# Performance work log

Measured on AMD Instinct MI355X. Metric: run time of the kernel, lower is better.

Reference implementation:

```python
import jax, jax.numpy as jnp
import numpy as np

B, A, M, N = 16, 98304, 32, 32  # batch, anchors, gt boxes per image, sample size
IMG = 512.0


def _make_boxes(key, prefix):
    """Valid [x1,y1,x2,y2] boxes inside a 512px image (x2>x1, y2>y1)."""
    k1, k2 = jax.random.split(key)
    xy = jax.random.uniform(k1, prefix + (2,), minval=0.0, maxval=IMG - 130.0)
    wh = jax.random.uniform(k2, prefix + (2,), minval=16.0, maxval=128.0)
    return jnp.concatenate([xy, xy + wh], axis=-1)


def setup_inputs() -> dict:
    key = jax.random.key(0)
    ks = jax.random.split(key, 4)
    classifications = jax.random.uniform(ks[0], (B, A, 2), minval=0.01, maxval=0.99)
    regressions = jax.random.normal(ks[1], (B, A, 4), dtype=jnp.float32)
    anchors = _make_boxes(ks[2], (1, A))
    ann_boxes = _make_boxes(ks[3], (B, M))
    annotations = jnp.concatenate([ann_boxes, jnp.zeros((B, M, 1))], axis=-1)
    w = jnp.ones((B, 4), dtype=jnp.float32)
    return {"classifications": classifications, "regressions": regressions,
            "anchors": anchors, "annotations": annotations, "w": w}


def _calc_iou(a, b):
    # a: [A,4] anchors, b: [M,4] gt boxes -> [A,M]
    area = (b[:, 2] - b[:, 0]) * (b[:, 3] - b[:, 1])  # [M]
    iw = jnp.minimum(a[:, 2:3], b[None, :, 2]) - jnp.maximum(a[:, 0:1], b[None, :, 0])
    ih = jnp.minimum(a[:, 3:4], b[None, :, 3]) - jnp.maximum(a[:, 1:2], b[None, :, 1])
    iw = jnp.clip(iw, 0.0)
    ih = jnp.clip(ih, 0.0)
    a_area = (a[:, 2] - a[:, 0]) * (a[:, 3] - a[:, 1])  # [A]
    ua = jnp.clip(a_area[:, None] + area[None, :] - iw * ih, 1e-8)
    return iw * ih / ua


def _per_image(cls_j, reg_j, anchor, ann_j, w_j, keys):
    nA = anchor.shape[0]
    cls_j = jnp.clip(cls_j, 1e-7, 1.0 - 1e-7)
    # class forced to 0, coords clamped to [0,512] (as in the torch module)
    bbox = jnp.clip(ann_j[:, :4], 0.0, IMG)
    iou = _calc_iou(anchor, bbox)                # [A, M]
    iou_max = iou.max(axis=1)
    iou_arg = iou.argmax(axis=1)

    # --- positive sampling: random subset of size min(N, count) via random top-k ---
    thresh = jnp.minimum(iou_max.max(), 0.7)
    pos_elig = iou_max >= thresh
    s_pos = jnp.where(pos_elig, jax.random.uniform(keys[0], (nA,), minval=0.1, maxval=1.0), -1.0)
    vpos, ipos = jax.lax.top_k(s_pos, N)
    keep_pos = vpos > 0.0                         # only eligible anchors
    pos_sel = jnp.zeros(nA, bool).at[ipos].set(keep_pos)
    K = keep_pos.sum()

    # --- negative sampling: random subset of size min(2N-K, count) ---
    neg_elig = (iou_max < 0.4) & (iou_max >= 0.1)
    s_neg = jnp.where(neg_elig, jax.random.uniform(keys[1], (nA,), minval=0.1, maxval=1.0), -1.0)
    vneg, ineg = jax.lax.top_k(s_neg, 2 * N)
    keep_neg = (vneg > 0.0) & (jnp.arange(2 * N) < (2 * N - K))
    neg_sel = jnp.zeros(nA, bool).at[ineg].set(keep_neg)

    # targets: positives -> [1,0] (class forced to 0), negatives -> [0,1], else -1 (ignore)
    t0 = jnp.where(pos_sel, 1.0, jnp.where(neg_sel, 0.0, -1.0))
    t1 = jnp.where(pos_sel, 0.0, jnp.where(neg_sel, 1.0, -1.0))
    targets = jnp.stack([t0, t1], axis=-1)       # [A,2]
    cls_loss = jnp.where(targets != -1.0, -(targets * jnp.log(cls_j)), 0.0).sum() / (2 * N)

    aw = anchor[:, 2] - anchor[:, 0]
    ah = anchor[:, 3] - anchor[:, 1]
    acx = anchor[:, 0] + 0.5 * aw
    acy = anchor[:, 1] + 0.5 * ah
    assigned = bbox[iou_arg]                     # [A,4]
    gw = assigned[:, 2] - assigned[:, 0]
    gh = assigned[:, 3] - assigned[:, 1]
    gcx = assigned[:, 0] + 0.5 * gw
    gcy = assigned[:, 1] + 0.5 * gh
    gw = jnp.maximum(gw, 1.0)
    gh = jnp.maximum(gh, 1.0)
    t = jnp.stack([(gcx - acx) / aw, (gcy - acy) / ah,
                   jnp.log(gw / aw), jnp.log(gh / ah)], axis=-1)
    t = t / jnp.array([0.1, 0.1, 0.2, 0.2], dtype=t.dtype)
    diff = jnp.abs(t - reg_j)
    sl1 = jnp.where(diff <= 1.0 / 9.0, 0.5 * 9.0 * diff * diff, diff - 0.5 / 9.0)
    reg_loss = (sl1 * pos_sel[:, None].astype(sl1.dtype)).sum() * w_j[0] / (2 * N)
    return cls_loss, reg_loss


def reference(classifications, regressions, anchors, annotations, w):
    anchor = anchors[0]
    bsz = classifications.shape[0]
    keys = jax.random.split(jax.random.key(42), bsz * 2).reshape(bsz, 2)
    cl, rl = jax.vmap(
        lambda c, r, a, wj, k: _per_image(c, r, anchor, a, wj, k)
    )(classifications, regressions, annotations, w, keys)
    return (jnp.mean(cl, keepdims=True), jnp.mean(rl, keepdims=True))
```

## Files before the change

kernel.cpp:

```cpp
#include <hip/hip_runtime.h>

#define NB 16
#define NA 98304
#define NM 32
#define NS 32
#define BLKI 48
#define BLKP 96
#define TARGET 256
#define GCAP 1024
#define BCAP 512

typedef unsigned int u32;
typedef unsigned long long u64;

static_assert(NA == BLKI * 256 * 8, "coverage iou");
static_assert(NA == BLKP * 256 * 4, "coverage push");

struct WS {
  u64   pos_key[NB * GCAP];
  u64   neg_key[NB * GCAP];
  float iou_max[NB * NA];
  float blk_max[NB * BLKI];
  int   blk_nneg[NB * BLKI];
  int   blk_npos[NB * BLKI];
  float thresh[NB], cut_pos[NB], cut_neg[NB];
  int   n_neg[NB], n_pos07[NB], ge07[NB];
  u32   keys[NB][4];
  int   pos_cnt[NB], neg_cnt[NB];
  u32   cls_bits[NB], reg_bits[NB];
  int   done;
};

__device__ __forceinline__ u32 rotl32(u32 v, int d) { return (v << d) | (v >> (32 - d)); }

__device__ __forceinline__ void threefry2x32(u32 k0, u32 k1, u32 x0, u32 x1, u32& o0, u32& o1) {
  u32 k2 = k0 ^ k1 ^ 0x1BD11BDAu;
  x0 += k0; x1 += k1;
  x0 += x1; x1 = rotl32(x1, 13); x1 ^= x0;
  x0 += x1; x1 = rotl32(x1, 15); x1 ^= x0;
  x0 += x1; x1 = rotl32(x1, 26); x1 ^= x0;
  x0 += x1; x1 = rotl32(x1, 6);  x1 ^= x0;
  x0 += k1; x1 += k2 + 1u;
  x0 += x1; x1 = rotl32(x1, 17); x1 ^= x0;
  x0 += x1; x1 = rotl32(x1, 29); x1 ^= x0;
  x0 += x1; x1 = rotl32(x1, 16); x1 ^= x0;
  x0 += x1; x1 = rotl32(x1, 24); x1 ^= x0;
  x0 += k2; x1 += k0 + 2u;
  x0 += x1; x1 = rotl32(x1, 13); x1 ^= x0;
  x0 += x1; x1 = rotl32(x1, 15); x1 ^= x0;
  x0 += x1; x1 = rotl32(x1, 26); x1 ^= x0;
  x0 += x1; x1 = rotl32(x1, 6);  x1 ^= x0;
  x0 += k0; x1 += k1 + 3u;
  x0 += x1; x1 = rotl32(x1, 17); x1 ^= x0;
  x0 += x1; x1 = rotl32(x1, 29); x1 ^= x0;
  x0 += x1; x1 = rotl32(x1, 16); x1 ^= x0;
  x0 += x1; x1 = rotl32(x1, 24); x1 ^= x0;
  x0 += k1; x1 += k2 + 4u;
  x0 += x1; x1 = rotl32(x1, 13); x1 ^= x0;
  x0 += x1; x1 = rotl32(x1, 15); x1 ^= x0;
  x0 += x1; x1 = rotl32(x1, 26); x1 ^= x0;
  x0 += x1; x1 = rotl32(x1, 6);  x1 ^= x0;
  x0 += k2; x1 += k0 + 5u;
  o0 = x0; o1 = x1;
}

__device__ __forceinline__ float tf_uniform(u32 k0, u32 k1, u32 idx) {
  u32 o0, o1;
  threefry2x32(k0, k1, 0u, idx, o0, o1);
  u32 bits = o0 ^ o1;
  float f = __uint_as_float((bits >> 9) | 0x3F800000u) - 1.0f;
  float u = __fadd_rn(__fmul_rn(f, (1.0f - 0.1f)), 0.1f);
  return fmaxf(0.1f, u);
}

__device__ __forceinline__ u64 pack_key(float u, u32 a) {
  return ((u64)__float_as_uint(u) << 32) | (u64)(u32)(~a);
}

__global__ __launch_bounds__(256) void k_iou(const float* __restrict__ anchors,
                                             const float* __restrict__ ann,
                                             WS* __restrict__ ws) {
  int b = blockIdx.y;
  int tid = threadIdx.x;
  int a0 = (blockIdx.x * 256 + tid) * 8;
  __shared__ float bx1[NM], by1[NM], bx2[NM], by2[NM], barea[NM];
  __shared__ float wmax[4];
  __shared__ int wneg[4], wpos[4];
  if (tid < NM) {
    int m = tid;
    const float* p = ann + ((size_t)b * NM + m) * 5;
    float x1 = fminf(fmaxf(p[0], 0.0f), 512.0f);
    float y1 = fminf(fmaxf(p[1], 0.0f), 512.0f);
    float x2 = fminf(fmaxf(p[2], 0.0f), 512.0f);
    float y2 = fminf(fmaxf(p[3], 0.0f), 512.0f);
    bx1[m] = x1; by1[m] = y1; bx2[m] = x2; by2[m] = y2;
    barea[m] = __fmul_rn(__fsub_rn(x2, x1), __fsub_rn(y2, y1));
  }
  __syncthreads();

  const float4* a4 = (const float4*)anchors;
  float4 ap[8];
  float aarea[8], bi[8], bu[8];
#pragma unroll
  for (int k = 0; k < 8; k++) {
    ap[k] = a4[a0 + k];
    aarea[k] = __fmul_rn(__fsub_rn(ap[k].z, ap[k].x), __fsub_rn(ap[k].w, ap[k].y));
    bi[k] = -1.0f;
    bu[k] = 1.0f;
  }
  for (int m = 0; m < NM; m++) {
    float x1 = bx1[m], y1 = by1[m], x2 = bx2[m], y2 = by2[m], ar = barea[m];
#pragma unroll
    for (int k = 0; k < 8; k++) {
      float iw = fmaxf(__fsub_rn(fminf(ap[k].z, x2), fmaxf(ap[k].x, x1)), 0.0f);
      float ih = fmaxf(__fsub_rn(fminf(ap[k].w, y2), fmaxf(ap[k].y, y1)), 0.0f);
      float inter = __fmul_rn(iw, ih);
      float ua = __fsub_rn(__fadd_rn(aarea[k], ar), inter);
      bool upd = __fmul_rn(inter, bu[k]) > __fmul_rn(bi[k], ua);
      bi[k] = upd ? inter : bi[k];
      bu[k] = upd ? ua : bu[k];
    }
  }
  float best[8];
#pragma unroll
  for (int k = 0; k < 8; k++) best[k] = __fdiv_rn(bi[k], bu[k]);

  size_t o = (size_t)b * NA + a0;
  *(float4*)&ws->iou_max[o]     = make_float4(best[0], best[1], best[2], best[3]);
  *(float4*)&ws->iou_max[o + 4] = make_float4(best[4], best[5], best[6], best[7]);

  float lmax = -1.0f;
  int cneg = 0, cpos = 0;
#pragma unroll
  for (int k = 0; k < 8; k++) {
    lmax = fmaxf(lmax, best[k]);
    cneg += (best[k] < 0.4f && best[k] >= 0.1f) ? 1 : 0;
    cpos += (best[k] >= 0.7f) ? 1 : 0;
  }
  for (int s = 32; s > 0; s >>= 1) {
    lmax = fmaxf(lmax, __shfl_xor(lmax, s));
    cneg += __shfl_xor(cneg, s);
    cpos += __shfl_xor(cpos, s);
  }
  int wid = tid >> 6;
  if ((tid & 63) == 0) { wmax[wid] = lmax; wneg[wid] = cneg; wpos[wid] = cpos; }
  __syncthreads();
  if (tid < 4) {
    lmax = wmax[tid]; cneg = wneg[tid]; cpos = wpos[tid];
    for (int s = 2; s > 0; s >>= 1) {
      lmax = fmaxf(lmax, __shfl_xor(lmax, s));
      cneg += __shfl_xor(cneg, s);
      cpos += __shfl_xor(cpos, s);
    }
    if (tid == 0) {
      int oo = b * BLKI + blockIdx.x;
      ws->blk_max[oo] = lmax;
      ws->blk_nneg[oo] = cneg;
      ws->blk_npos[oo] = cpos;
    }
  }
}

__global__ __launch_bounds__(256) void k_stats(WS* __restrict__ ws) {
  int tid = threadIdx.x;
  int b = tid >> 4, l = tid & 15;
  float m = -1.0f;
  int nn = 0, np = 0;
  for (int i = l; i < BLKI; i += 16) {
    m = fmaxf(m, ws->blk_max[b * BLKI + i]);
    nn += ws->blk_nneg[b * BLKI + i];
    np += ws->blk_npos[b * BLKI + i];
  }
  for (int s = 8; s > 0; s >>= 1) {
    m = fmaxf(m, __shfl_xor(m, s));
    nn += __shfl_xor(nn, s);
    np += __shfl_xor(np, s);
  }
  if (l == 0) {
    ws->thresh[b] = fminf(m, 0.7f);
    int ge = (m >= 0.7f) ? 1 : 0;
    ws->ge07[b] = ge;
    ws->n_neg[b] = nn;
    ws->n_pos07[b] = np;
    ws->cut_neg[b] = (nn <= TARGET) ? -1.0f : (1.0f - 0.9f * ((float)TARGET / (float)nn));
    ws->cut_pos[b] = (ge && np > TARGET) ? (1.0f - 0.9f * ((float)TARGET / (float)np)) : -1.0f;
    ws->pos_cnt[b] = 0;
    ws->neg_cnt[b] = 0;
    u32 o0, o1;
    threefry2x32(0u, 42u, 0u, (u32)(2 * b), o0, o1);
    ws->keys[b][0] = o0; ws->keys[b][1] = o1;
    threefry2x32(0u, 42u, 0u, (u32)(2 * b + 1), o0, o1);
    ws->keys[b][2] = o0; ws->keys[b][3] = o1;
  }
  if (tid == 0) ws->done = 0;
}

__global__ __launch_bounds__(256) void k_push(WS* __restrict__ ws) {
  int b = blockIdx.y, tid = threadIdx.x;
  int a0 = (blockIdx.x * 256 + tid) * 4;
  __shared__ u64 pbuf[BCAP], nbuf[BCAP];
  __shared__ int pcnt, ncnt, pbase, nbase;
  if (tid == 0) { pcnt = 0; ncnt = 0; }
  __syncthreads();
  float thresh = ws->thresh[b];
  float cp = ws->cut_pos[b], cn = ws->cut_neg[b];
  u32 k0 = ws->keys[b][0], k1 = ws->keys[b][1];
  u32 k2 = ws->keys[b][2], k3 = ws->keys[b][3];
  float4 im4 = *(const float4*)&ws->iou_max[(size_t)b * NA + a0];
  float imv[4] = {im4.x, im4.y, im4.z, im4.w};
#pragma unroll
  for (int k = 0; k < 4; k++) {
    float im = imv[k];
    u32 a = (u32)(a0 + k);
    if (im >= thresh) {
      float u = tf_uniform(k0, k1, a);
      if (u >= cp) {
        int p = atomicAdd(&pcnt, 1);
        if (p < BCAP) pbuf[p] = pack_key(u, a);
      }
    }
    if (im < 0.4f && im >= 0.1f) {
      float u = tf_uniform(k2, k3, a);
      if (u >= cn) {
        int p = atomicAdd(&ncnt, 1);
        if (p < BCAP) nbuf[p] = pack_key(u, a);
      }
    }
  }
  __syncthreads();
  if (tid == 0) {
    pbase = (pcnt > 0) ? atomicAdd(&ws->pos_cnt[b], pcnt) : 0;
    nbase = (ncnt > 0) ? atomicAdd(&ws->neg_cnt[b], ncnt) : 0;
  }
  __syncthreads();
  int pc = min(pcnt, BCAP), nc = min(ncnt, BCAP);
  for (int i = tid; i < pc; i += 256) { int g = pbase + i; if (g < GCAP) ws->pos_key[b * GCAP + g] = pbuf[i]; }
  for (int i = tid; i < nc; i += 256) { int g = nbase + i; if (g < GCAP) ws->neg_key[b * GCAP + g] = nbuf[i]; }
}

__global__ __launch_bounds__(256) void k_select(const float* __restrict__ cls,
                                                const float* __restrict__ reg,
                                                const float* __restrict__ anchors,
                                                const float* __restrict__ ann,
                                                const float* __restrict__ w,
                                                WS* __restrict__ ws,
                                                float* __restrict__ out) {
  int b = blockIdx.x, tid = threadIdx.x;
  __shared__ u64 pk[GCAP], nk[GCAP];
  __shared__ float bx1[NM], by1[NM], bx2[NM], by2[NM], barea[NM];
  __shared__ int selp[NS], seln[2 * NS];
  __shared__ float tpos[NS], treg[NS], tneg[2 * NS];

  if (tid < NM) {
    int m = tid;
    const float* p = ann + ((size_t)b * NM + m) * 5;
    float x1 = fminf(fmaxf(p[0], 0.0f), 512.0f);
    float y1 = fminf(fmaxf(p[1], 0.0f), 512.0f);
    float x2 = fminf(fmaxf(p[2], 0.0f), 512.0f);
    float y2 = fminf(fmaxf(p[3], 0.0f), 512.0f);
    bx1[m] = x1; by1[m] = y1; bx2[m] = x2; by2[m] = y2;
    barea[m] = __fmul_rn(__fsub_rn(x2, x1), __fsub_rn(y2, y1));
  }

  int mp = min(ws->pos_cnt[b], GCAP);
  int mn = min(ws->neg_cnt[b], GCAP);
  int n_pos = ws->ge07[b] ? ws->n_pos07[b] : ws->pos_cnt[b];
  int n_neg = ws->n_neg[b];
  int K = min(NS, n_pos);
  int rp = min(K, mp);
  int rn = min(min(2 * NS - K, n_neg), mn);

  int mpad = (mp + 255) & ~255;
  int npad = (mn + 255) & ~255;
  for (int i = tid; i < mpad; i += 256) pk[i] = (i < mp) ? ws->pos_key[b * GCAP + i] : 0ull;
  for (int i = tid; i < npad; i += 256) nk[i] = (i < mn) ? ws->neg_key[b * GCAP + i] : 0ull;
  if (tid < NS) { tpos[tid] = 0.0f; treg[tid] = 0.0f; }
  if (tid < 2 * NS) tneg[tid] = 0.0f;
  __syncthreads();

  {
    u64 ck[GCAP / 256]; int cr[GCAP / 256];
    int nc = mpad >> 8;
#pragma unroll
    for (int c = 0; c < GCAP / 256; c++) { ck[c] = 0; cr[c] = 0; }
    for (int c = 0; c < nc; c++) ck[c] = pk[tid + (c << 8)];
    for (int j = 0; j < mp; j++) {
      u64 v = pk[j];
#pragma unroll
      for (int c = 0; c < GCAP / 256; c++) cr[c] += (v > ck[c]) ? 1 : 0;
    }
    for (int c = 0; c < nc; c++)
      if (ck[c] != 0 && cr[c] < rp) selp[cr[c]] = (int)(~(u32)ck[c]);
  }
  {
    u64 ck[GCAP / 256]; int cr[GCAP / 256];
    int nc = npad >> 8;
#pragma unroll
    for (int c = 0; c < GCAP / 256; c++) { ck[c] = 0; cr[c] = 0; }
    for (int c = 0; c < nc; c++) ck[c] = nk[tid + (c << 8)];
    for (int j = 0; j < mn; j++) {
      u64 v = nk[j];
#pragma unroll
      for (int c = 0; c < GCAP / 256; c++) cr[c] += (v > ck[c]) ? 1 : 0;
    }
    for (int c = 0; c < nc; c++)
      if (ck[c] != 0 && cr[c] < rn) seln[cr[c]] = (int)(~(u32)ck[c]);
  }
  __syncthreads();

  const float PLO = 1e-7f;
  const float PHI = (float)(1.0 - 1e-7);
  if (tid < rp) {
    int a = selp[tid];
    float p = cls[((size_t)b * NA + a) * 2 + 0];
    p = fminf(fmaxf(p, PLO), PHI);
    tpos[tid] = -logf(p);
    float4 apf = ((const float4*)anchors)[a];
    float ax1 = apf.x, ay1 = apf.y, ax2 = apf.z, ay2 = apf.w;
    float aarea = __fmul_rn(__fsub_rn(ax2, ax1), __fsub_rn(ay2, ay1));
    float bestv = -1.0f; int bestm = 0;
    for (int m = 0; m < NM; m++) {
      float iw = fmaxf(__fsub_rn(fminf(ax2, bx2[m]), fmaxf(ax1, bx1[m])), 0.0f);
      float ih = fmaxf(__fsub_rn(fminf(ay2, by2[m]), fmaxf(ay1, by1[m])), 0.0f);
      float inter = __fmul_rn(iw, ih);
      float ua = fmaxf(__fsub_rn(__fadd_rn(aarea, barea[m]), inter), 1e-8f);
      float v = __fdiv_rn(inter, ua);
      if (v > bestv) { bestv = v; bestm = m; }
    }
    float aw_ = __fsub_rn(ax2, ax1), ah_ = __fsub_rn(ay2, ay1);
    float acx = __fadd_rn(ax1, __fmul_rn(0.5f, aw_));
    float acy = __fadd_rn(ay1, __fmul_rn(0.5f, ah_));
    float gx1 = bx1[bestm], gy1 = by1[bestm], gx2 = bx2[bestm], gy2 = by2[bestm];
    float gw = __fsub_rn(gx2, gx1), gh = __fsub_rn(gy2, gy1);
    float gcx = __fadd_rn(gx1, __fmul_rn(0.5f, gw));
    float gcy = __fadd_rn(gy1, __fmul_rn(0.5f, gh));
    gw = fmaxf(gw, 1.0f); gh = fmaxf(gh, 1.0f);
    float t0 = __fdiv_rn(__fdiv_rn(__fsub_rn(gcx, acx), aw_), 0.1f);
    float t1 = __fdiv_rn(__fdiv_rn(__fsub_rn(gcy, acy), ah_), 0.1f);
    float t2 = __fdiv_rn(logf(__fdiv_rn(gw, aw_)), 0.2f);
    float t3 = __fdiv_rn(logf(__fdiv_rn(gh, ah_)), 0.2f);
    const float* rg = reg + ((size_t)b * NA + a) * 4;
    float tt[4] = {t0, t1, t2, t3};
    float s = 0.0f;
#pragma unroll
    for (int c = 0; c < 4; c++) {
      float d = fabsf(__fsub_rn(tt[c], rg[c]));
      float q = (d <= (float)(1.0 / 9.0)) ? __fmul_rn(__fmul_rn(4.5f, d), d)
                                          : __fsub_rn(d, (float)(0.5 / 9.0));
      s = __fadd_rn(s, q);
    }
    treg[tid] = s;
  }
  if (tid < rn) {
    int a = seln[tid];
    bool ispos = false;
    for (int i = 0; i < rp; i++) if (selp[i] == a) ispos = true;
    if (!ispos) {
      float p = cls[((size_t)b * NA + a) * 2 + 1];
      p = fminf(fmaxf(p, PLO), PHI);
      tneg[tid] = -logf(p);
    }
  }
  __syncthreads();
  if (tid == 0) {
    float cs = 0.0f;
    for (int i = 0; i < NS; i++) cs = __fadd_rn(cs, tpos[i]);
    for (int i = 0; i < 2 * NS; i++) cs = __fadd_rn(cs, tneg[i]);
    float rs = 0.0f;
    for (int i = 0; i < NS; i++) rs = __fadd_rn(rs, treg[i]);
    float ci = __fdiv_rn(cs, 64.0f);
    float ri = __fdiv_rn(__fmul_rn(rs, w[b * 4 + 0]), 64.0f);
    atomicExch(&ws->cls_bits[b], __float_as_uint(ci));
    atomicExch(&ws->reg_bits[b], __float_as_uint(ri));
    __threadfence();
    int old = atomicAdd(&ws->done, 1);
    if (old == NB - 1) {
      float c = 0.0f, r = 0.0f;
      for (int j = 0; j < NB; j++) {
        c = __fadd_rn(c, __uint_as_float(atomicOr(&ws->cls_bits[j], 0u)));
        r = __fadd_rn(r, __uint_as_float(atomicOr(&ws->reg_bits[j], 0u)));
      }
      out[0] = __fdiv_rn(c, 16.0f);
      out[1] = __fdiv_rn(r, 16.0f);
    }
  }
}

extern "C" void kernel_launch(void* const* d_in, const int* in_sizes, int n_in,
                              void* d_out, int out_size, void* d_ws, size_t ws_size,
                              hipStream_t stream) {
  const float* cls = (const float*)d_in[0];
  const float* reg = (const float*)d_in[1];
  const float* anchors = (const float*)d_in[2];
  const float* ann = (const float*)d_in[3];
  const float* w = (const float*)d_in[4];
  float* out = (float*)d_out;
  if (ws_size < sizeof(WS)) return;
  WS* ws = (WS*)d_ws;

  hipLaunchKernelGGL(k_iou, dim3(BLKI, NB), dim3(256), 0, stream, anchors, ann, ws);
  hipLaunchKernelGGL(k_stats, dim3(1), dim3(256), 0, stream, ws);
  hipLaunchKernelGGL(k_push, dim3(BLKP, NB), dim3(256), 0, stream, ws);
  hipLaunchKernelGGL(k_select, dim3(NB), dim3(256), 0, stream, cls, reg, anchors, ann, w, ws, out);
}
```

Measured before the change: 90.09 us.

## Fold stats kernel into push/select and shrink per-thread IoU work

Removes the single-block k_stats launch. Each k_push block now recomputes the per-image threshold, cut values and RNG keys from the per-block partials, and k_select recomputes the counts it needs. The counter reset moves into k_iou. k_iou now handles 4 anchors per thread instead of 8 across twice as many blocks, which raises parallelism, and it reads each box as a float4 from shared memory. The final cross-block reduction uses release/acquire atomics instead of atomicExch plus a fence and atomicOr reads. The cost is redundant small reductions in every push block, in exchange for one fewer launch and one fewer serialization point.

```diff
diff --git a/kernel.cpp b/kernel.cpp
--- a/kernel.cpp
+++ b/kernel.cpp
@@ -4,8 +4,7 @@
 #define NA 98304
 #define NM 32
 #define NS 32
-#define BLKI 48
-#define BLKP 96
+#define BLKI 96
 #define TARGET 256
 #define GCAP 1024
 #define BCAP 512
@@ -13,8 +12,7 @@
 typedef unsigned int u32;
 typedef unsigned long long u64;
 
-static_assert(NA == BLKI * 256 * 8, "coverage iou");
-static_assert(NA == BLKP * 256 * 4, "coverage push");
+static_assert(NA == BLKI * 256 * 4, "coverage");
 
 struct WS {
   u64   pos_key[NB * GCAP];
@@ -23,9 +21,6 @@
   float blk_max[NB * BLKI];
   int   blk_nneg[NB * BLKI];
   int   blk_npos[NB * BLKI];
-  float thresh[NB], cut_pos[NB], cut_neg[NB];
-  int   n_neg[NB], n_pos07[NB], ge07[NB];
-  u32   keys[NB][4];
   int   pos_cnt[NB], neg_cnt[NB];
   u32   cls_bits[NB], reg_bits[NB];
   int   done;
@@ -77,43 +72,64 @@
   return ((u64)__float_as_uint(u) << 32) | (u64)(u32)(~a);
 }
 
+__device__ __forceinline__ void reduce_stats(const WS* ws, int b, int tid,
+                                             float& m, int& nn, int& np) {
+  m = -1.0f; nn = 0; np = 0;
+  for (int i = tid; i < BLKI; i += 64) {
+    m = fmaxf(m, ws->blk_max[b * BLKI + i]);
+    nn += ws->blk_nneg[b * BLKI + i];
+    np += ws->blk_npos[b * BLKI + i];
+  }
+  for (int s = 32; s > 0; s >>= 1) {
+    m = fmaxf(m, __shfl_xor(m, s));
+    nn += __shfl_xor(nn, s);
+    np += __shfl_xor(np, s);
+  }
+}
+
 __global__ __launch_bounds__(256) void k_iou(const float* __restrict__ anchors,
                                              const float* __restrict__ ann,
                                              WS* __restrict__ ws) {
   int b = blockIdx.y;
   int tid = threadIdx.x;
-  int a0 = (blockIdx.x * 256 + tid) * 8;
-  __shared__ float bx1[NM], by1[NM], bx2[NM], by2[NM], barea[NM];
+  int a0 = (blockIdx.x * 256 + tid) * 4;
+  __shared__ float4 sbox[NM];
+  __shared__ float sarea[NM];
   __shared__ float wmax[4];
   __shared__ int wneg[4], wpos[4];
   if (tid < NM) {
-    int m = tid;
-    const float* p = ann + ((size_t)b * NM + m) * 5;
+    const float* p = ann + ((size_t)b * NM + tid) * 5;
     float x1 = fminf(fmaxf(p[0], 0.0f), 512.0f);
     float y1 = fminf(fmaxf(p[1], 0.0f), 512.0f);
     float x2 = fminf(fmaxf(p[2], 0.0f), 512.0f);
     float y2 = fminf(fmaxf(p[3], 0.0f), 512.0f);
-    bx1[m] = x1; by1[m] = y1; bx2[m] = x2; by2[m] = y2;
-    barea[m] = __fmul_rn(__fsub_rn(x2, x1), __fsub_rn(y2, y1));
+    sbox[tid] = make_float4(x1, y1, x2, y2);
+    sarea[tid] = __fmul_rn(__fsub_rn(x2, x1), __fsub_rn(y2, y1));
+  }
+  if (blockIdx.x == 0 && tid == 0) {
+    ws->pos_cnt[b] = 0;
+    ws->neg_cnt[b] = 0;
+    if (b == 0) ws->done = 0;
   }
   __syncthreads();
 
   const float4* a4 = (const float4*)anchors;
-  float4 ap[8];
-  float aarea[8], bi[8], bu[8];
-#pragma unroll
-  for (int k = 0; k < 8; k++) {
+  float4 ap[4];
+  float aarea[4], bi[4], bu[4];
+#pragma unroll
+  for (int k = 0; k < 4; k++) {
     ap[k] = a4[a0 + k];
     aarea[k] = __fmul_rn(__fsub_rn(ap[k].z, ap[k].x), __fsub_rn(ap[k].w, ap[k].y));
     bi[k] = -1.0f;
     bu[k] = 1.0f;
   }
   for (int m = 0; m < NM; m++) {
-    float x1 = bx1[m], y1 = by1[m], x2 = bx2[m], y2 = by2[m], ar = barea[m];
-#pragma unroll
-    for (int k = 0; k < 8; k++) {
-      float iw = fmaxf(__fsub_rn(fminf(ap[k].z, x2), fmaxf(ap[k].x, x1)), 0.0f);
-      float ih = fmaxf(__fsub_rn(fminf(ap[k].w, y2), fmaxf(ap[k].y, y1)), 0.0f);
+    float4 bx = sbox[m];
+    float ar = sarea[m];
+#pragma unroll
+    for (int k = 0; k < 4; k++) {
+      float iw = fmaxf(__fsub_rn(fminf(ap[k].z, bx.z), fmaxf(ap[k].x, bx.x)), 0.0f);
+      float ih = fmaxf(__fsub_rn(fminf(ap[k].w, bx.w), fmaxf(ap[k].y, bx.y)), 0.0f);
       float inter = __fmul_rn(iw, ih);
       float ua = __fsub_rn(__fadd_rn(aarea[k], ar), inter);
       bool upd = __fmul_rn(inter, bu[k]) > __fmul_rn(bi[k], ua);
@@ -121,19 +137,15 @@
       bu[k] = upd ? ua : bu[k];
     }
   }
-  float best[8];
-#pragma unroll
-  for (int k = 0; k < 8; k++) best[k] = __fdiv_rn(bi[k], bu[k]);
-
-  size_t o = (size_t)b * NA + a0;
-  *(float4*)&ws->iou_max[o]     = make_float4(best[0], best[1], best[2], best[3]);
-  *(float4*)&ws->iou_max[o + 4] = make_float4(best[4], best[5], best[6], best[7]);
-
-  float lmax = -1.0f;
+  float best[4];
+#pragma unroll
+  for (int k = 0; k < 4; k++) best[k] = __fdiv_rn(bi[k], bu[k]);
+  *(float4*)&ws->iou_max[(size_t)b * NA + a0] = make_float4(best[0], best[1], best[2], best[3]);
+
+  float lmax = fmaxf(fmaxf(best[0], best[1]), fmaxf(best[2], best[3]));
   int cneg = 0, cpos = 0;
 #pragma unroll
-  for (int k = 0; k < 8; k++) {
-    lmax = fmaxf(lmax, best[k]);
+  for (int k = 0; k < 4; k++) {
     cneg += (best[k] < 0.4f && best[k] >= 0.1f) ? 1 : 0;
     cpos += (best[k] >= 0.7f) ? 1 : 0;
   }
@@ -153,46 +165,12 @@
       cpos += __shfl_xor(cpos, s);
     }
     if (tid == 0) {
-      int oo = b * BLKI + blockIdx.x;
-      ws->blk_max[oo] = lmax;
-      ws->blk_nneg[oo] = cneg;
-      ws->blk_npos[oo] = cpos;
-    }
-  }
-}
-
-__global__ __launch_bounds__(256) void k_stats(WS* __restrict__ ws) {
-  int tid = threadIdx.x;
-  int b = tid >> 4, l = tid & 15;
-  float m = -1.0f;
-  int nn = 0, np = 0;
-  for (int i = l; i < BLKI; i += 16) {
-    m = fmaxf(m, ws->blk_max[b * BLKI + i]);
-    nn += ws->blk_nneg[b * BLKI + i];
-    np += ws->blk_npos[b * BLKI + i];
-  }
-  for (int s = 8; s > 0; s >>= 1) {
-    m = fmaxf(m, __shfl_xor(m, s));
-    nn += __shfl_xor(nn, s);
-    np += __shfl_xor(np, s);
-  }
-  if (l == 0) {
-    ws->thresh[b] = fminf(m, 0.7f);
-    int ge = (m >= 0.7f) ? 1 : 0;
-    ws->ge07[b] = ge;
-    ws->n_neg[b] = nn;
-    ws->n_pos07[b] = np;
-    ws->cut_neg[b] = (nn <= TARGET) ? -1.0f : (1.0f - 0.9f * ((float)TARGET / (float)nn));
-    ws->cut_pos[b] = (ge && np > TARGET) ? (1.0f - 0.9f * ((float)TARGET / (float)np)) : -1.0f;
-    ws->pos_cnt[b] = 0;
-    ws->neg_cnt[b] = 0;
-    u32 o0, o1;
-    threefry2x32(0u, 42u, 0u, (u32)(2 * b), o0, o1);
-    ws->keys[b][0] = o0; ws->keys[b][1] = o1;
-    threefry2x32(0u, 42u, 0u, (u32)(2 * b + 1), o0, o1);
-    ws->keys[b][2] = o0; ws->keys[b][3] = o1;
-  }
-  if (tid == 0) ws->done = 0;
+      int o = b * BLKI + blockIdx.x;
+      ws->blk_max[o] = lmax;
+      ws->blk_nneg[o] = cneg;
+      ws->blk_npos[o] = cpos;
+    }
+  }
 }
 
 __global__ __launch_bounds__(256) void k_push(WS* __restrict__ ws) {
@@ -200,12 +178,27 @@
   int a0 = (blockIdx.x * 256 + tid) * 4;
   __shared__ u64 pbuf[BCAP], nbuf[BCAP];
   __shared__ int pcnt, ncnt, pbase, nbase;
+  __shared__ float s_thresh, s_cp, s_cn;
+  __shared__ u32 s_keys[4];
   if (tid == 0) { pcnt = 0; ncnt = 0; }
-  __syncthreads();
-  float thresh = ws->thresh[b];
-  float cp = ws->cut_pos[b], cn = ws->cut_neg[b];
-  u32 k0 = ws->keys[b][0], k1 = ws->keys[b][1];
-  u32 k2 = ws->keys[b][2], k3 = ws->keys[b][3];
+  if (tid < 64) {
+    float m; int nn, np;
+    reduce_stats(ws, b, tid, m, nn, np);
+    if (tid == 0) {
+      s_thresh = fminf(m, 0.7f);
+      int ge = (m >= 0.7f) ? 1 : 0;
+      s_cn = (nn <= TARGET) ? -1.0f : (1.0f - 0.9f * ((float)TARGET / (float)nn));
+      s_cp = (ge && np > TARGET) ? (1.0f - 0.9f * ((float)TARGET / (float)np)) : -1.0f;
+      u32 o0, o1;
+      threefry2x32(0u, 42u, 0u, (u32)(2 * b), o0, o1);
+      s_keys[0] = o0; s_keys[1] = o1;
+      threefry2x32(0u, 42u, 0u, (u32)(2 * b + 1), o0, o1);
+      s_keys[2] = o0; s_keys[3] = o1;
+    }
+  }
+  __syncthreads();
+  float thresh = s_thresh, cp = s_cp, cn = s_cn;
+  u32 k0 = s_keys[0], k1 = s_keys[1], k2 = s_keys[2], k3 = s_keys[3];
   float4 im4 = *(const float4*)&ws->iou_max[(size_t)b * NA + a0];
   float imv[4] = {im4.x, im4.y, im4.z, im4.w};
 #pragma unroll
@@ -250,26 +243,29 @@
   __shared__ float bx1[NM], by1[NM], bx2[NM], by2[NM], barea[NM];
   __shared__ int selp[NS], seln[2 * NS];
   __shared__ float tpos[NS], treg[NS], tneg[2 * NS];
+  __shared__ int s_npos, s_nneg;
 
   if (tid < NM) {
-    int m = tid;
-    const float* p = ann + ((size_t)b * NM + m) * 5;
+    const float* p = ann + ((size_t)b * NM + tid) * 5;
     float x1 = fminf(fmaxf(p[0], 0.0f), 512.0f);
     float y1 = fminf(fmaxf(p[1], 0.0f), 512.0f);
     float x2 = fminf(fmaxf(p[2], 0.0f), 512.0f);
     float y2 = fminf(fmaxf(p[3], 0.0f), 512.0f);
-    bx1[m] = x1; by1[m] = y1; bx2[m] = x2; by2[m] = y2;
-    barea[m] = __fmul_rn(__fsub_rn(x2, x1), __fsub_rn(y2, y1));
+    bx1[tid] = x1; by1[tid] = y1; bx2[tid] = x2; by2[tid] = y2;
+    barea[tid] = __fmul_rn(__fsub_rn(x2, x1), __fsub_rn(y2, y1));
+  }
+  if (tid >= 64 && tid < 128) {
+    float m; int nn, np;
+    reduce_stats(ws, b, tid - 64, m, nn, np);
+    if (tid == 64) {
+      int ge = (m >= 0.7f) ? 1 : 0;
+      s_npos = ge ? np : ws->pos_cnt[b];
+      s_nneg = nn;
+    }
   }
 
   int mp = min(ws->pos_cnt[b], GCAP);
   int mn = min(ws->neg_cnt[b], GCAP);
-  int n_pos = ws->ge07[b] ? ws->n_pos07[b] : ws->pos_cnt[b];
-  int n_neg = ws->n_neg[b];
-  int K = min(NS, n_pos);
-  int rp = min(K, mp);
-  int rn = min(min(2 * NS - K, n_neg), mn);
-
   int mpad = (mp + 255) & ~255;
   int npad = (mn + 255) & ~255;
   for (int i = tid; i < mpad; i += 256) pk[i] = (i < mp) ? ws->pos_key[b * GCAP + i] : 0ull;
@@ -277,6 +273,10 @@
   if (tid < NS) { tpos[tid] = 0.0f; treg[tid] = 0.0f; }
   if (tid < 2 * NS) tneg[tid] = 0.0f;
   __syncthreads();
+
+  int K = min(NS, s_npos);
+  int rp = min(K, mp);
+  int rn = min(min(2 * NS - K, s_nneg), mn);
 
   {
     u64 ck[GCAP / 256]; int cr[GCAP / 256];
@@ -370,15 +370,21 @@
     for (int i = 0; i < NS; i++) rs = __fadd_rn(rs, treg[i]);
     float ci = __fdiv_rn(cs, 64.0f);
     float ri = __fdiv_rn(__fmul_rn(rs, w[b * 4 + 0]), 64.0f);
-    atomicExch(&ws->cls_bits[b], __float_as_uint(ci));
-    atomicExch(&ws->reg_bits[b], __float_as_uint(ri));
-    __threadfence();
-    int old = atomicAdd(&ws->done, 1);
+    __hip_atomic_store(&ws->cls_bits[b], __float_as_uint(ci), __ATOMIC_RELEASE, __HIP_MEMORY_SCOPE_AGENT);
+    __hip_atomic_store(&ws->reg_bits[b], __float_as_uint(ri), __ATOMIC_RELEASE, __HIP_MEMORY_SCOPE_AGENT);
+    int old = __hip_atomic_fetch_add(&ws->done, 1, __ATOMIC_ACQ_REL, __HIP_MEMORY_SCOPE_AGENT);
     if (old == NB - 1) {
+      u32 cb[NB], rb[NB];
+#pragma unroll
+      for (int j = 0; j < NB; j++) {
+        cb[j] = __hip_atomic_load(&ws->cls_bits[j], __ATOMIC_RELAXED, __HIP_MEMORY_SCOPE_AGENT);
+        rb[j] = __hip_atomic_load(&ws->reg_bits[j], __ATOMIC_RELAXED, __HIP_MEMORY_SCOPE_AGENT);
+      }
       float c = 0.0f, r = 0.0f;
+#pragma unroll
       for (int j = 0; j < NB; j++) {
-        c = __fadd_rn(c, __uint_as_float(atomicOr(&ws->cls_bits[j], 0u)));
-        r = __fadd_rn(r, __uint_as_float(atomicOr(&ws->reg_bits[j], 0u)));
+        c = __fadd_rn(c, __uint_as_float(cb[j]));
+        r = __fadd_rn(r, __uint_as_float(rb[j]));
       }
       out[0] = __fdiv_rn(c, 16.0f);
       out[1] = __fdiv_rn(r, 16.0f);
@@ -399,7 +405,6 @@
   WS* ws = (WS*)d_ws;
 
   hipLaunchKernelGGL(k_iou, dim3(BLKI, NB), dim3(256), 0, stream, anchors, ann, ws);
-  hipLaunchKernelGGL(k_stats, dim3(1), dim3(256), 0, stream, ws);
-  hipLaunchKernelGGL(k_push, dim3(BLKP, NB), dim3(256), 0, stream, ws);
+  hipLaunchKernelGGL(k_push, dim3(BLKI, NB), dim3(256), 0, stream, ws);
   hipLaunchKernelGGL(k_select, dim3(NB), dim3(256), 0, stream, cls, reg, anchors, ann, w, ws, out);
 }
```

Measured after the change: 76.08 us. 1.18x faster.
